# Optimization experiments

Hardware: AMD Instinct MI355X
Metric: run time of the kernel (lower is better)

The kernel has to match this reference:

```python
import jax, jax.numpy as jnp
import numpy as np
from jax import lax

H = 1024  # hidden_size
L = 2     # num_layers


def gru_cell(x, h, Wih, Whh, bih, bhh):
    # PyTorch GRU gate order: r, z, n
    gi = x @ Wih.T + bih          # [B, 3H]
    gh = h @ Whh.T + bhh          # [B, 3H]
    ir, iz, inn = jnp.split(gi, 3, axis=-1)
    hr, hz, hn = jnp.split(gh, 3, axis=-1)
    r = jax.nn.sigmoid(ir + hr)
    z = jax.nn.sigmoid(iz + hz)
    n = jnp.tanh(inn + r * hn)
    return (1.0 - z) * n + z * h


def stacked_step(h, x_t, layers):
    # h: [L, B, H]; x_t: [B, in]; layers: list of (Wih, Whh, bih, bhh)
    hs = []
    inp = x_t
    for l, (Wih, Whh, bih, bhh) in enumerate(layers):
        hl = gru_cell(inp, h[l], Wih, Whh, bih, bhh)
        hs.append(hl)
        inp = hl
    return jnp.stack(hs), inp  # new hidden stack, top-layer output


def run_gru_seq(x_seq, h0, layers):
    # x_seq: [B, S, in] -> scan over time
    def step(h, x_t):
        h_new, out = stacked_step(h, x_t, layers)
        return h_new, out
    h_final, outs = lax.scan(step, h0, jnp.transpose(x_seq, (1, 0, 2)))
    return outs[-1], h_final  # last-timestep top-layer output [B, H]


def setup_inputs() -> dict:
    key = jax.random.key(0)
    ks = jax.random.split(key, 10)
    B, S = 128, 256

    def xavier(k, shape):
        fan_out, fan_in = shape
        std = np.sqrt(2.0 / (fan_in + fan_out))
        return jax.random.normal(k, shape, dtype=jnp.float32) * std

    inp = {
        "x": jax.random.normal(ks[0], (B, S), dtype=jnp.float32),
        "h0": jax.random.uniform(ks[1], (L, B, H), dtype=jnp.float32) * 0.01,
        "Wih0": xavier(ks[2], (3 * H, 1)),
        "Whh0": xavier(ks[3], (3 * H, H)),
        "bih0": jnp.zeros((3 * H,), jnp.float32),
        "bhh0": jnp.zeros((3 * H,), jnp.float32),
        "Wih1": xavier(ks[4], (3 * H, H)),
        "Whh1": xavier(ks[5], (3 * H, H)),
        "bih1": jnp.zeros((3 * H,), jnp.float32),
        "bhh1": jnp.zeros((3 * H,), jnp.float32),
        "fc_w": jax.random.uniform(ks[6], (1, H), jnp.float32, -1.0 / np.sqrt(H), 1.0 / np.sqrt(H)),
        "fc_b": jax.random.uniform(ks[7], (1,), jnp.float32, -1.0 / np.sqrt(H), 1.0 / np.sqrt(H)),
        "forcast_length": 8,
    }
    return inp


def reference(x, h0, Wih0, Whh0, bih0, bhh0, Wih1, Whh1, bih1, bhh1, fc_w, fc_b, forcast_length):
    layers = [(Wih0, Whh0, bih0, bhh0), (Wih1, Whh1, bih1, bhh1)]

    # forecast step i=0: full conditioning sequence
    out0, h = run_gru_seq(x[..., None], h0, layers)   # [B, H], [L, B, H]
    y0 = out0 @ fc_w.T + fc_b                          # [B, 1]

    def fstep(carry, _):
        xc, hc = carry                                 # xc: [B, 1]
        h_new, out = stacked_step(hc, xc, layers)
        y = out @ fc_w.T + fc_b                        # [B, 1]
        return (y, h_new), y[:, 0]

    (y_last, h_final), ys = lax.scan(fstep, (y0, h), None, length=forcast_length - 1)
    forcast_out = jnp.concatenate([y0[:, 0][None, :], ys], axis=0)  # [F, B]
    return jnp.mean(forcast_out, axis=0), h_final
```

## Files before the change

### kernel.cpp

```cpp
#include <hip/hip_runtime.h>

#define NB 128
#define NH 1024
#define NS 256
#define NF 8
#define NBLK 192
#define NTH 512
#define AG  __HIP_MEMORY_SCOPE_AGENT

#define GLOBL 0
#define XARR  32
#define XRELL (32*9)
#define XCPY  (32*17)
#define XCNT  (32*25)
#define INITL (32*33)

typedef _Float16 half_t;
typedef _Float16 f16x8 __attribute__((ext_vector_type(8)));
typedef float f32x4 __attribute__((ext_vector_type(4)));
typedef unsigned long long u64;

struct GP {
    const float *x, *hin, *Wih0, *Whh0, *bih0, *bhh0, *Wih1, *Whh1, *bih1, *bhh1, *fcw, *fcb;
    float *gib0, *gib1, *ys, *out;
    half_t *h0b0, *h0b1, *h1b0, *h1b1;
    char *reg;
    unsigned *bar;
};

__device__ __forceinline__ float fast_sigmoid(float x) { return 1.0f / (1.0f + __expf(-x)); }
__device__ __forceinline__ float fast_tanh(float x) {
    float e = __expf(2.0f * x);
    return (e - 1.0f) / (e + 1.0f);
}

__device__ __forceinline__ u64 ldu64(const void* p) {
    return __hip_atomic_load((const u64*)p, __ATOMIC_RELAXED, AG);
}
__device__ __forceinline__ void stu64(void* p, u64 v) {
    __hip_atomic_store((u64*)p, v, __ATOMIC_RELAXED, AG);
}
__device__ __forceinline__ float ldf32(const float* p) {
    return __hip_atomic_load(p, __ATOMIC_RELAXED, AG);
}
__device__ __forceinline__ void stf32(float* p, float v) {
    __hip_atomic_store(p, v, __ATOMIC_RELAXED, AG);
}
__device__ __forceinline__ unsigned aadd(unsigned* p, unsigned v) {
    return __hip_atomic_fetch_add(p, v, __ATOMIC_RELAXED, AG);
}
__device__ __forceinline__ unsigned ald(const unsigned* p) {
    return __hip_atomic_load(p, __ATOMIC_RELAXED, AG);
}

__global__ void k_init(const float* __restrict__ hin, half_t* __restrict__ h0h,
                       half_t* __restrict__ h1h) {
    int i = blockIdx.x * 256 + threadIdx.x;
    h0h[i] = (half_t)hin[i];
    h1h[i] = (half_t)hin[NB * NH + i];
}

__global__ __launch_bounds__(NTH)
void k_gru(GP p) {
    extern __shared__ char lds[];
    const int tid = threadIdx.x;
    const int l   = tid & 63;
    const int wv  = tid >> 6;
    const int bid = blockIdx.x;
    const int role = (bid < 64) ? 0 : (bid < 128 ? 1 : 2);
    const int bc   = bid & 63;
    const int colbase = bc * 16;
    float* hl  = (float*)(lds + 98304);
    int* meta  = (int*)(lds + 106496);
    unsigned* bar = p.bar;

    {
        const float* Wsrc = (role == 0) ? p.Whh0 : ((role == 1) ? p.Wih1 : p.Whh1);
        for (int i = tid; i < 12288; i += NTH) {
            int row = i >> 8, j = i & 255;
            int g = row >> 4, r = row & 15;
            float4 v = *(const float4*)(Wsrc + (size_t)(g * NH + colbase + r) * NH + j * 4);
            union { half_t h[4]; uint2 u; } cv;
            cv.h[0] = (half_t)v.x; cv.h[1] = (half_t)v.y;
            cv.h[2] = (half_t)v.z; cv.h[3] = (half_t)v.w;
            *(uint2*)(lds + (row * 2048 + ((j * 8) ^ ((row & 7) << 4)))) = cv.u;
        }
        if (role != 1) {
            const float* hsrc = p.hin + (role == 2 ? NB * NH : 0);
            for (int i = tid; i < NB * 16; i += NTH) {
                int b = i >> 4, cl = i & 15;
                hl[i] = hsrc[(size_t)b * NH + colbase + cl];
            }
        }
    }

    if (tid == 0) {
        unsigned x;
        asm volatile("s_getreg_b32 %0, hwreg(HW_REG_XCC_ID)" : "=s"(x));
        x &= 7;
        unsigned r = aadd(bar + XCNT + x * 32, 1u);
        asm volatile("s_waitcnt vmcnt(0)" ::: "memory");
        aadd(bar + INITL, 1u);
        while (ald(bar + INITL) < NBLK) __builtin_amdgcn_s_sleep(1);
        int nn = 0, cnt = 0;
        for (int k = 0; k < 8; ++k) {
            unsigned c = ald(bar + XCNT + k * 32);
            if (c) ++cnt;
            if (k == (int)x) nn = (int)c;
        }
        meta[0] = (int)x; meta[1] = (int)r; meta[2] = nn; meta[3] = cnt;
    }
    __syncthreads();
    const int xcd_  = meta[0];
    const int rank_ = meta[1];
    const int n_    = meta[2];
    const int nx_   = meta[3];

    const int cloc = l & 15;
    const int c = colbase + cloc;
    float bi_[3] = {0,0,0}, bh_[3] = {0,0,0}, wx_[3] = {0,0,0};
    if (role == 0) {
        #pragma unroll
        for (int g = 0; g < 3; ++g) {
            bi_[g] = p.bih0[g * NH + c]; bh_[g] = p.bhh0[g * NH + c];
            wx_[g] = p.Wih0[g * NH + c];
        }
    } else if (role == 2) {
        #pragma unroll
        for (int g = 0; g < 3; ++g) {
            bi_[g] = p.bih1[g * NH + c]; bh_[g] = p.bhh1[g * NH + c];
        }
    }

    const int rbase[3] = { cloc * 2048, (16 + cloc) * 2048, (32 + cloc) * 2048 };
    const int rmask = (cloc & 7) << 4;
    const int kb0 = (l >> 4) << 4;
    const int arow = wv * 16 + cloc;
    const int b0base = wv * 16 + ((l >> 4) << 2);
    const int aloff = (l >> 4) * 2048 + arow * 16;

    auto gbar = [&](unsigned t) {
        __syncthreads();
        if (tid == 0) {
            asm volatile("s_waitcnt vmcnt(0)" ::: "memory");
            aadd(bar + XARR + xcd_ * 32, 1u);
            if (rank_ == 0) {
                while (ald(bar + XARR + xcd_ * 32) < (unsigned)n_ * t) __builtin_amdgcn_s_sleep(1);
                aadd(bar + GLOBL, 1u);
                while (ald(bar + GLOBL) < (unsigned)nx_ * t) __builtin_amdgcn_s_sleep(1);
                __hip_atomic_store(bar + XRELL + xcd_ * 32, t, __ATOMIC_RELAXED, AG);
            } else {
                while (ald(bar + XRELL + xcd_ * 32) < t) __builtin_amdgcn_s_sleep(1);
            }
        }
        __syncthreads();
        asm volatile("buffer_inv" ::: "memory");
    };

    auto xcopy = [&](const half_t* h0s, const half_t* h1s, int slot) {
        char* dst = p.reg + ((size_t)(xcd_ * 2 + slot)) * 524288;
        for (int idx = rank_ * 512 + tid; idx < 32768; idx += n_ * 512) {
            int which = idx >> 14, kq = (idx >> 7) & 127, row = idx & 127;
            const half_t* s = (which ? h1s : h0s) + row * 1024 + kq * 8;
            union { u64 u[2]; uint4 v; } t;
            t.u[0] = ldu64(s);
            t.u[1] = ldu64(s + 4);
            *(uint4*)(dst + which * 262144 + (size_t)(kq * 128 + row) * 16) = t.v;
        }
    };
    auto csync = [&](unsigned ct) {
        __syncthreads();
        if (tid == 0) {
            asm volatile("s_waitcnt vmcnt(0)" ::: "memory");
            aadd(bar + XCPY + xcd_ * 32, 1u);
            while (ald(bar + XCPY + xcd_ * 32) < (unsigned)n_ * ct) __builtin_amdgcn_s_sleep(1);
        }
        __syncthreads();
    };

    auto do_gemm = [&](const char* regA, f32x4 (&acc)[3]) {
        const char* ap = regA + aloff;
        #pragma unroll 8
        for (int ks = 0; ks < 32; ++ks) {
            f16x8 a = *(const f16x8*)(ap + (size_t)ks * 8192);
            int kb = ks * 64 + kb0;
            #pragma unroll
            for (int g = 0; g < 3; ++g) {
                f16x8 bf = *(const f16x8*)(lds + rbase[g] + (kb ^ rmask));
                acc[g] = __builtin_amdgcn_mfma_f32_16x16x32_f16(a, bf, acc[g], 0, 0, 0);
            }
        }
    };

    auto pack_store_h = [&](half_t* hw, int b, float hn) {
        unsigned v = (unsigned)__builtin_bit_cast(unsigned short, (half_t)hn);
        unsigned o = __shfl_xor(v, 1);
        unsigned pair = (l & 1) ? (o | (v << 16)) : (v | (o << 16));
        unsigned p2 = __shfl_xor(pair, 2);
        u64 quad = (l & 2) ? (((u64)pair << 32) | p2) : ((u64)pair | ((u64)p2 << 32));
        if ((l & 3) == 0) stu64(hw + (size_t)b * NH + (c & ~3), quad);
    };

    auto l0_epi = [&](const float xv[4], f32x4 (&acc)[3], half_t* hw) {
        #pragma unroll
        for (int q = 0; q < 4; ++q) {
            int b = b0base + q;
            float gh0 = acc[0][q] + bh_[0];
            float gh1 = acc[1][q] + bh_[1];
            float gh2 = acc[2][q] + bh_[2];
            float r_ = fast_sigmoid(xv[q] * wx_[0] + bi_[0] + gh0);
            float z_ = fast_sigmoid(xv[q] * wx_[1] + bi_[1] + gh1);
            float n_2 = fast_tanh(xv[q] * wx_[2] + bi_[2] + r_ * gh2);
            float hp = hl[b * 16 + cloc];
            float hn = (1.0f - z_) * n_2 + z_ * hp;
            hl[b * 16 + cloc] = hn;
            pack_store_h(hw, b, hn);
        }
    };

    auto gi_epi = [&](f32x4 (&acc)[3], float* gw) {
        #pragma unroll
        for (int g = 0; g < 3; ++g) {
            union { f32x4 v; u64 u[2]; } t; t.v = acc[g];
            float* dst = gw + ((size_t)g * NH + c) * NB + b0base;
            stu64(dst, t.u[0]);
            stu64(dst + 2, t.u[1]);
        }
    };

    auto gh_epi = [&](f32x4 (&acc)[3], const f32x4 gv[3], half_t* hw) {
        #pragma unroll
        for (int q = 0; q < 4; ++q) {
            int b = b0base + q;
            float gh0 = acc[0][q] + bh_[0];
            float gh1 = acc[1][q] + bh_[1];
            float gh2 = acc[2][q] + bh_[2];
            float r_ = fast_sigmoid(gv[0][q] + bi_[0] + gh0);
            float z_ = fast_sigmoid(gv[1][q] + bi_[1] + gh1);
            float n_2 = fast_tanh(gv[2][q] + bi_[2] + r_ * gh2);
            float hp = hl[b * 16 + cloc];
            float hn = (1.0f - z_) * n_2 + z_ * hp;
            hl[b * 16 + cloc] = hn;
            pack_store_h(hw, b, hn);
        }
    };

    auto load_gi = [&](const float* gr, f32x4 (&gv)[3]) {
        #pragma unroll
        for (int g = 0; g < 3; ++g) {
            union { f32x4 v; u64 u[2]; } t;
            const float* src = gr + ((size_t)g * NH + c) * NB + b0base;
            t.u[0] = ldu64(src);
            t.u[1] = ldu64(src + 2);
            gv[g] = t.v;
        }
    };

    auto do_fc = [&](const char* regH1, float* dst) {
        if (bid == 0) {
            int row = tid >> 2, part = tid & 3;
            const char* hp = regH1 + (size_t)row * 16;
            const float4* wp = (const float4*)p.fcw;
            float s = 0.0f;
            #pragma unroll 8
            for (int kk = 0; kk < 32; ++kk) {
                int kq = part * 32 + kk;
                union { f16x8 v; half_t h[8]; } a;
                a.v = *(const f16x8*)(hp + (size_t)kq * 2048);
                float4 w0 = wp[kq * 2], w1 = wp[kq * 2 + 1];
                s += (float)a.h[0]*w0.x + (float)a.h[1]*w0.y + (float)a.h[2]*w0.z + (float)a.h[3]*w0.w
                   + (float)a.h[4]*w1.x + (float)a.h[5]*w1.y + (float)a.h[6]*w1.z + (float)a.h[7]*w1.w;
            }
            s += __shfl_xor(s, 1);
            s += __shfl_xor(s, 2);
            if (part == 0) stf32(dst + row, s + p.fcb[0]);
        }
    };

    unsigned tgt = 0, ctgt = 0;
    int cur0 = 0, cur1 = 0, gcur = 0;
    f32x4 zero4 = {0.f, 0.f, 0.f, 0.f};

    auto COPY = [&]() {
        ++ctgt;
        int slot = (int)(ctgt & 1);
        xcopy(cur0 ? p.h0b1 : p.h0b0, cur1 ? p.h1b1 : p.h1b0, slot);
        csync(ctgt);
        return p.reg + ((size_t)(xcd_ * 2 + slot)) * 524288;
    };

    for (int ph = 0; ph < NS + 2; ++ph) {
        const char* regB = COPY();
        if (role == 0 && ph < NS) {
            float xv[4];
            #pragma unroll
            for (int q = 0; q < 4; ++q) xv[q] = ldf32(p.x + (size_t)(b0base + q) * NS + ph);
            f32x4 acc[3] = {zero4, zero4, zero4};
            do_gemm(regB, acc);
            l0_epi(xv, acc, cur0 ? p.h0b0 : p.h0b1);
        } else if (role == 1 && ph >= 1 && ph <= NS) {
            f32x4 acc[3] = {zero4, zero4, zero4};
            do_gemm(regB, acc);
            gi_epi(acc, gcur ? p.gib0 : p.gib1);
        } else if (role == 2 && ph >= 2) {
            f32x4 gv[3];
            load_gi(gcur ? p.gib1 : p.gib0, gv);
            f32x4 acc[3] = {zero4, zero4, zero4};
            do_gemm(regB + 262144, acc);
            gh_epi(acc, gv, cur1 ? p.h1b0 : p.h1b1);
        }
        ++tgt; gbar(tgt);
        if (ph < NS) cur0 ^= 1;
        if (ph >= 1 && ph <= NS) gcur ^= 1;
        if (ph >= 2) cur1 ^= 1;
    }

    for (int i = 1; i < NF; ++i) {
        const char* regB = COPY();
        do_fc(regB + 262144, p.ys + (i - 1) * NB);
        ++tgt; gbar(tgt);

        regB = COPY();
        if (role == 0) {
            float xv[4];
            #pragma unroll
            for (int q = 0; q < 4; ++q) xv[q] = ldf32(p.ys + (i - 1) * NB + b0base + q);
            f32x4 acc[3] = {zero4, zero4, zero4};
            do_gemm(regB, acc);
            l0_epi(xv, acc, cur0 ? p.h0b0 : p.h0b1);
        }
        ++tgt; gbar(tgt); cur0 ^= 1;

        regB = COPY();
        if (role == 1) {
            f32x4 acc[3] = {zero4, zero4, zero4};
            do_gemm(regB, acc);
            gi_epi(acc, gcur ? p.gib0 : p.gib1);
        }
        ++tgt; gbar(tgt); gcur ^= 1;

        regB = COPY();
        if (role == 2) {
            f32x4 gv[3];
            load_gi(gcur ? p.gib1 : p.gib0, gv);
            f32x4 acc[3] = {zero4, zero4, zero4};
            do_gemm(regB + 262144, acc);
            gh_epi(acc, gv, cur1 ? p.h1b0 : p.h1b1);
        }
        ++tgt; gbar(tgt); cur1 ^= 1;
    }
    {
        const char* regB = COPY();
        do_fc(regB + 262144, p.ys + 7 * NB);
        ++tgt; gbar(tgt);
    }

    if (bid == 0 && tid < NB) {
        float s = 0.0f;
        #pragma unroll
        for (int k = 0; k < NF; ++k) s += ldf32(p.ys + k * NB + tid);
        p.out[tid] = s * 0.125f;
    }
    if (role != 1) {
        float* ob = p.out + NB + (role == 2 ? (size_t)NB * NH : 0);
        for (int i = tid; i < NB * 16; i += NTH) {
            int b = i >> 4, cl = i & 15;
            ob[(size_t)b * NH + colbase + cl] = hl[i];
        }
    }
}

extern "C" void kernel_launch(void* const* d_in, const int* in_sizes, int n_in,
                              void* d_out, int out_size, void* d_ws, size_t ws_size,
                              hipStream_t stream)
{
    GP p;
    p.x    = (const float*)d_in[0];
    p.hin  = (const float*)d_in[1];
    p.Wih0 = (const float*)d_in[2];
    p.Whh0 = (const float*)d_in[3];
    p.bih0 = (const float*)d_in[4];
    p.bhh0 = (const float*)d_in[5];
    p.Wih1 = (const float*)d_in[6];
    p.Whh1 = (const float*)d_in[7];
    p.bih1 = (const float*)d_in[8];
    p.bhh1 = (const float*)d_in[9];
    p.fcw  = (const float*)d_in[10];
    p.fcb  = (const float*)d_in[11];
    p.out  = (float*)d_out;

    char* ws = (char*)d_ws;
    p.bar  = (unsigned*)ws;                      ws += 8192;
    p.h0b0 = (half_t*)ws;                        ws += 262144;
    p.h0b1 = (half_t*)ws;                        ws += 262144;
    p.h1b0 = (half_t*)ws;                        ws += 262144;
    p.h1b1 = (half_t*)ws;                        ws += 262144;
    p.gib0 = (float*)ws;                         ws += 1572864;
    p.gib1 = (float*)ws;                         ws += 1572864;
    p.ys   = (float*)ws;                         ws += 4096;
    ws = (char*)(((size_t)ws + 4095) & ~(size_t)4095);
    p.reg  = ws;                                 ws += 8 * 2 * 524288;

    hipMemsetAsync(p.bar, 0, 8192, stream);
    k_init<<<512, 256, 0, stream>>>(p.hin, p.h0b0, p.h1b0);

    void* args[] = { &p };
    if (hipLaunchCooperativeKernel((void*)k_gru, dim3(NBLK), dim3(NTH), args,
                                   106752, stream) != hipSuccess) {
        (void)hipGetLastError();
        k_gru<<<dim3(NBLK), dim3(NTH), 106752, stream>>>(p);
    }
}
```

Before: 4.004 ms.

## Fuse FC projection into layer-1 epilogue and streamline grid barrier

The separate FC phase run by block 0, with its own copy and grid barrier per forecast step, is removed. The top-layer epilogue now computes the FC dot product itself, using shuffle reductions and atomicAdd into ys, which is pre-seeded with the bias in the init kernel. This drops eight grid barriers and copy rounds. The grid barrier is also reworked: per-XCD arrival uses non-returning L2 atomics and polling via returning atomics, and all blocks wait on a single global release counter bumped by the last arriver. The risks are float atomic ordering nondeterminism and memory-visibility correctness, since the explicit s_waitcnt before arrival is gone.

```diff
diff --git a/kernel.cpp b/kernel.cpp
--- a/kernel.cpp
+++ b/kernel.cpp
@@ -9,11 +9,11 @@
 #define AG  __HIP_MEMORY_SCOPE_AGENT
 
 #define GLOBL 0
-#define XARR  32
-#define XRELL (32*9)
-#define XCPY  (32*17)
-#define XCNT  (32*25)
-#define INITL (32*33)
+#define RELL  64
+#define INITL 128
+#define XCNT  192
+#define XARR  512
+#define XCPY  1024
 
 typedef _Float16 half_t;
 typedef _Float16 f16x8 __attribute__((ext_vector_type(8)));
@@ -43,9 +43,6 @@
 __device__ __forceinline__ float ldf32(const float* p) {
     return __hip_atomic_load(p, __ATOMIC_RELAXED, AG);
 }
-__device__ __forceinline__ void stf32(float* p, float v) {
-    __hip_atomic_store(p, v, __ATOMIC_RELAXED, AG);
-}
 __device__ __forceinline__ unsigned aadd(unsigned* p, unsigned v) {
     return __hip_atomic_fetch_add(p, v, __ATOMIC_RELAXED, AG);
 }
@@ -53,11 +50,26 @@
     return __hip_atomic_load(p, __ATOMIC_RELAXED, AG);
 }
 
+__device__ __forceinline__ void l2add(unsigned* p, unsigned v) {
+    asm volatile("global_atomic_add %0, %1, off" :: "v"(p), "v"(v) : "memory");
+}
+__device__ __forceinline__ unsigned l2add_rtn(unsigned* p, unsigned v) {
+    unsigned ret;
+    asm volatile("global_atomic_add %0, %1, %2, off sc0\n\ts_waitcnt vmcnt(0)"
+                 : "=v"(ret) : "v"(p), "v"(v) : "memory");
+    return ret;
+}
+
 __global__ void k_init(const float* __restrict__ hin, half_t* __restrict__ h0h,
-                       half_t* __restrict__ h1h) {
+                       half_t* __restrict__ h1h, const float* __restrict__ fcb,
+                       float* __restrict__ ys) {
     int i = blockIdx.x * 256 + threadIdx.x;
     h0h[i] = (half_t)hin[i];
     h1h[i] = (half_t)hin[NB * NH + i];
+    if (blockIdx.x == 0) {
+        float fb = fcb[0];
+        for (int j = threadIdx.x; j < NF * NB; j += 256) ys[j] = fb;
+    }
 }
 
 __global__ __launch_bounds__(NTH)
@@ -118,7 +130,7 @@
 
     const int cloc = l & 15;
     const int c = colbase + cloc;
-    float bi_[3] = {0,0,0}, bh_[3] = {0,0,0}, wx_[3] = {0,0,0};
+    float bi_[3] = {0,0,0}, bh_[3] = {0,0,0}, wx_[3] = {0,0,0}, fcwv = 0.f;
     if (role == 0) {
         #pragma unroll
         for (int g = 0; g < 3; ++g) {
@@ -130,6 +142,7 @@
         for (int g = 0; g < 3; ++g) {
             bi_[g] = p.bih1[g * NH + c]; bh_[g] = p.bhh1[g * NH + c];
         }
+        fcwv = p.fcw[c];
     }
 
     const int rbase[3] = { cloc * 2048, (16 + cloc) * 2048, (32 + cloc) * 2048 };
@@ -142,16 +155,14 @@
     auto gbar = [&](unsigned t) {
         __syncthreads();
         if (tid == 0) {
-            asm volatile("s_waitcnt vmcnt(0)" ::: "memory");
-            aadd(bar + XARR + xcd_ * 32, 1u);
+            l2add(bar + XARR + xcd_ * 32, 1u);
             if (rank_ == 0) {
-                while (ald(bar + XARR + xcd_ * 32) < (unsigned)n_ * t) __builtin_amdgcn_s_sleep(1);
-                aadd(bar + GLOBL, 1u);
-                while (ald(bar + GLOBL) < (unsigned)nx_ * t) __builtin_amdgcn_s_sleep(1);
-                __hip_atomic_store(bar + XRELL + xcd_ * 32, t, __ATOMIC_RELAXED, AG);
-            } else {
-                while (ald(bar + XRELL + xcd_ * 32) < t) __builtin_amdgcn_s_sleep(1);
+                while (l2add_rtn(bar + XARR + xcd_ * 32, 0u) < (unsigned)n_ * t)
+                    __builtin_amdgcn_s_sleep(1);
+                unsigned old = aadd(bar + GLOBL, 1u);
+                if (old == (unsigned)nx_ * t - 1u) aadd(bar + RELL, 1u);
             }
+            while (ald(bar + RELL) < t) __builtin_amdgcn_s_sleep(1);
         }
         __syncthreads();
         asm volatile("buffer_inv" ::: "memory");
@@ -171,9 +182,9 @@
     auto csync = [&](unsigned ct) {
         __syncthreads();
         if (tid == 0) {
-            asm volatile("s_waitcnt vmcnt(0)" ::: "memory");
-            aadd(bar + XCPY + xcd_ * 32, 1u);
-            while (ald(bar + XCPY + xcd_ * 32) < (unsigned)n_ * ct) __builtin_amdgcn_s_sleep(1);
+            l2add(bar + XCPY + xcd_ * 32, 1u);
+            while (l2add_rtn(bar + XCPY + xcd_ * 32, 0u) < (unsigned)n_ * ct)
+                __builtin_amdgcn_s_sleep(1);
         }
         __syncthreads();
     };
@@ -228,7 +239,8 @@
         }
     };
 
-    auto gh_epi = [&](f32x4 (&acc)[3], const f32x4 gv[3], half_t* hw) {
+    auto gh_epi = [&](f32x4 (&acc)[3], const f32x4 gv[3], half_t* hw, float* ydst) {
+        float hn4[4];
         #pragma unroll
         for (int q = 0; q < 4; ++q) {
             int b = b0base + q;
@@ -241,7 +253,22 @@
             float hp = hl[b * 16 + cloc];
             float hn = (1.0f - z_) * n_2 + z_ * hp;
             hl[b * 16 + cloc] = hn;
+            hn4[q] = hn;
             pack_store_h(hw, b, hn);
+        }
+        if (ydst) {
+            float s0 = hn4[0] * fcwv, s1 = hn4[1] * fcwv, s2 = hn4[2] * fcwv, s3 = hn4[3] * fcwv;
+            #pragma unroll
+            for (int m = 1; m < 16; m <<= 1) {
+                s0 += __shfl_xor(s0, m); s1 += __shfl_xor(s1, m);
+                s2 += __shfl_xor(s2, m); s3 += __shfl_xor(s3, m);
+            }
+            if (cloc == 0) {
+                atomicAdd(ydst + b0base, s0);
+                atomicAdd(ydst + b0base + 1, s1);
+                atomicAdd(ydst + b0base + 2, s2);
+                atomicAdd(ydst + b0base + 3, s3);
+            }
         }
     };
 
@@ -256,27 +283,6 @@
         }
     };
 
-    auto do_fc = [&](const char* regH1, float* dst) {
-        if (bid == 0) {
-            int row = tid >> 2, part = tid & 3;
-            const char* hp = regH1 + (size_t)row * 16;
-            const float4* wp = (const float4*)p.fcw;
-            float s = 0.0f;
-            #pragma unroll 8
-            for (int kk = 0; kk < 32; ++kk) {
-                int kq = part * 32 + kk;
-                union { f16x8 v; half_t h[8]; } a;
-                a.v = *(const f16x8*)(hp + (size_t)kq * 2048);
-                float4 w0 = wp[kq * 2], w1 = wp[kq * 2 + 1];
-                s += (float)a.h[0]*w0.x + (float)a.h[1]*w0.y + (float)a.h[2]*w0.z + (float)a.h[3]*w0.w
-                   + (float)a.h[4]*w1.x + (float)a.h[5]*w1.y + (float)a.h[6]*w1.z + (float)a.h[7]*w1.w;
-            }
-            s += __shfl_xor(s, 1);
-            s += __shfl_xor(s, 2);
-            if (part == 0) stf32(dst + row, s + p.fcb[0]);
-        }
-    };
-
     unsigned tgt = 0, ctgt = 0;
     int cur0 = 0, cur1 = 0, gcur = 0;
     f32x4 zero4 = {0.f, 0.f, 0.f, 0.f};
@@ -307,7 +313,7 @@
             load_gi(gcur ? p.gib1 : p.gib0, gv);
             f32x4 acc[3] = {zero4, zero4, zero4};
             do_gemm(regB + 262144, acc);
-            gh_epi(acc, gv, cur1 ? p.h1b0 : p.h1b1);
+            gh_epi(acc, gv, cur1 ? p.h1b0 : p.h1b1, (ph == NS + 1) ? p.ys : nullptr);
         }
         ++tgt; gbar(tgt);
         if (ph < NS) cur0 ^= 1;
@@ -317,10 +323,6 @@
 
     for (int i = 1; i < NF; ++i) {
         const char* regB = COPY();
-        do_fc(regB + 262144, p.ys + (i - 1) * NB);
-        ++tgt; gbar(tgt);
-
-        regB = COPY();
         if (role == 0) {
             float xv[4];
             #pragma unroll
@@ -345,14 +347,9 @@
             load_gi(gcur ? p.gib1 : p.gib0, gv);
             f32x4 acc[3] = {zero4, zero4, zero4};
             do_gemm(regB + 262144, acc);
-            gh_epi(acc, gv, cur1 ? p.h1b0 : p.h1b1);
+            gh_epi(acc, gv, cur1 ? p.h1b0 : p.h1b1, p.ys + i * NB);
         }
         ++tgt; gbar(tgt); cur1 ^= 1;
-    }
-    {
-        const char* regB = COPY();
-        do_fc(regB + 262144, p.ys + 7 * NB);
-        ++tgt; gbar(tgt);
     }
 
     if (bid == 0 && tid < NB) {
@@ -402,7 +399,7 @@
     p.reg  = ws;                                 ws += 8 * 2 * 524288;
 
     hipMemsetAsync(p.bar, 0, 8192, stream);
-    k_init<<<512, 256, 0, stream>>>(p.hin, p.h0b0, p.h1b0);
+    k_init<<<512, 256, 0, stream>>>(p.hin, p.h0b0, p.h1b0, p.fcb, p.ys);
 
     void* args[] = { &p };
     if (hipLaunchCooperativeKernel((void*)k_gru, dim3(NBLK), dim3(NTH), args,
```

Result: faster. 3.316 ms (-17.2%).
